# Kernel optimization log

Measured on AMD Instinct MI355X. Metric: run time of the kernel, lower is better.

## Reference

```python
import jax, jax.numpy as jnp
import numpy as np

N_EMBD = 1024
N_HEAD = 16
HEAD = N_EMBD // N_HEAD
D_FF = 4 * N_EMBD
B, T = 2, 2048


def setup_inputs() -> dict:
    key = jax.random.key(0)
    ks = jax.random.split(key, 12)
    s = 0.02
    return {
        "x": jax.random.normal(ks[0], (B, T, N_EMBD), jnp.float32),
        "Wq": jax.random.normal(ks[1], (N_EMBD, N_EMBD), jnp.float32) * s,
        "bq": jnp.zeros((N_EMBD,), jnp.float32),
        "Wk": jax.random.normal(ks[2], (N_EMBD, N_EMBD), jnp.float32) * s,
        "bk": jnp.zeros((N_EMBD,), jnp.float32),
        "Wv": jax.random.normal(ks[3], (N_EMBD, N_EMBD), jnp.float32) * s,
        "bv": jnp.zeros((N_EMBD,), jnp.float32),
        "Wo": jax.random.normal(ks[4], (N_EMBD, N_EMBD), jnp.float32) * s,
        "bo": jnp.zeros((N_EMBD,), jnp.float32),
        "W1": jax.random.normal(ks[5], (N_EMBD, D_FF), jnp.float32) * s,
        "b1": jnp.zeros((D_FF,), jnp.float32),
        "W2": jax.random.normal(ks[6], (D_FF, N_EMBD), jnp.float32) * s,
        "b2": jnp.zeros((N_EMBD,), jnp.float32),
        "g1": jnp.ones((N_EMBD,), jnp.float32),
        "be1": jnp.zeros((N_EMBD,), jnp.float32),
        "g2": jnp.ones((N_EMBD,), jnp.float32),
        "be2": jnp.zeros((N_EMBD,), jnp.float32),
    }


def _layernorm(x, g, b, eps=1e-3):
    # keras LayerNormalization default epsilon=1e-3
    mu = jnp.mean(x, axis=-1, keepdims=True)
    var = jnp.mean(jnp.square(x - mu), axis=-1, keepdims=True)
    return (x - mu) * jax.lax.rsqrt(var + eps) * g + b


def _attention(h, Wq, bq, Wk, bk, Wv, bv, Wo, bo):
    b, t, _ = h.shape
    q = (h @ Wq + bq).reshape(b, t, N_HEAD, HEAD)
    k = (h @ Wk + bk).reshape(b, t, N_HEAD, HEAD)
    v = (h @ Wv + bv).reshape(b, t, N_HEAD, HEAD)
    scores = jnp.einsum("bthd,bshd->bhts", q, k) / jnp.sqrt(jnp.float32(HEAD))
    causal = jnp.tril(jnp.ones((t, t), bool))
    scores = jnp.where(causal, scores, -jnp.inf)
    w = jax.nn.softmax(scores, axis=-1)  # dropout is identity in eval
    ctx = jnp.einsum("bhts,bshd->bthd", w, v).reshape(b, t, N_EMBD)
    return ctx @ Wo + bo


def reference(x, Wq, bq, Wk, bk, Wv, bv, Wo, bo, W1, b1, W2, b2, g1, be1, g2, be2):
    x = x + _attention(_layernorm(x, g1, be1), Wq, bq, Wk, bk, Wv, bv, Wo, bo)
    h = _layernorm(x, g2, be2)
    ff = jax.nn.relu(h @ W1 + b1) @ W2 + b2
    return x + ff
```

## Files before the change

### kernel.cpp

```cpp
#include <hip/hip_runtime.h>

typedef __bf16 bf16;
typedef __attribute__((ext_vector_type(8))) __bf16 bf16x8;
typedef __attribute__((ext_vector_type(4))) __bf16 bf16x4;
typedef __attribute__((ext_vector_type(4))) float f32x4;

#define MFMA16(A, B, C) __builtin_amdgcn_mfma_f32_16x16x32_bf16(A, B, C, 0, 0, 0)

#define GLOAD16(gp, lp)                                          \
  __builtin_amdgcn_global_load_lds(                              \
      (const __attribute__((address_space(1))) void*)(gp),       \
      (__attribute__((address_space(3))) void*)(lp), 16, 0, 0)

__device__ __forceinline__ float fexp2(float x) {
#if __has_builtin(__builtin_amdgcn_exp2f)
  return __builtin_amdgcn_exp2f(x);
#else
  float r;
  asm("v_exp_f32 %0, %1" : "=v"(r) : "v"(x));
  return r;
#endif
}

#define QSCL 0.18033688011112042f

__global__ __launch_bounds__(256) void transpose_cvt_kernel(
    const float* __restrict__ in, bf16* __restrict__ out, int K, int N)
{
  __shared__ float tile[32][33];
  const int kt = blockIdx.y * 32;
  const int nt = blockIdx.x * 32;
  const int tx = threadIdx.x, ty = threadIdx.y;
#pragma unroll
  for (int j = 0; j < 4; ++j)
    tile[ty + j * 8][tx] = in[(size_t)(kt + ty + j * 8) * N + nt + tx];
  __syncthreads();
#pragma unroll
  for (int j = 0; j < 4; ++j)
    out[(size_t)(nt + ty + j * 8) * K + kt + tx] = (bf16)tile[tx][ty + j * 8];
}

__global__ __launch_bounds__(256) void ln_kernel(
    const float* __restrict__ in, const float* __restrict__ gamma,
    const float* __restrict__ beta, bf16* __restrict__ out)
{
  const int row = blockIdx.x;
  const int t = threadIdx.x;
  const float4 v = ((const float4*)(in + (size_t)row * 1024))[t];
  float s = v.x + v.y + v.z + v.w;
  float sq = v.x * v.x + v.y * v.y + v.z * v.z + v.w * v.w;
#pragma unroll
  for (int m = 1; m < 64; m <<= 1) {
    s += __shfl_xor(s, m);
    sq += __shfl_xor(sq, m);
  }
  __shared__ float ssum[4], ssq[4];
  const int w = t >> 6;
  if ((t & 63) == 0) { ssum[w] = s; ssq[w] = sq; }
  __syncthreads();
  s = ssum[0] + ssum[1] + ssum[2] + ssum[3];
  sq = ssq[0] + ssq[1] + ssq[2] + ssq[3];
  const float mu = s * (1.0f / 1024.0f);
  const float var = sq * (1.0f / 1024.0f) - mu * mu;
  const float rs = rsqrtf(var + 1e-3f);
  const float4 g = ((const float4*)gamma)[t];
  const float4 b = ((const float4*)beta)[t];
  bf16x4 o;
  o[0] = (bf16)((v.x - mu) * rs * g.x + b.x);
  o[1] = (bf16)((v.y - mu) * rs * g.y + b.y);
  o[2] = (bf16)((v.z - mu) * rs * g.z + b.z);
  o[3] = (bf16)((v.w - mu) * rs * g.w + b.w);
  *(bf16x4*)(out + (size_t)row * 1024 + t * 4) = o;
}

template <int BN, int BK, int EPI>
__global__ __launch_bounds__(256) void gemm_bt(
    const bf16* __restrict__ A, const bf16* __restrict__ Bt,
    const float* __restrict__ bias0, const float* __restrict__ bias1,
    const float* __restrict__ bias2, const float* __restrict__ resid,
    bf16* __restrict__ out0, bf16* __restrict__ out1, bf16* __restrict__ out2,
    float* __restrict__ outf, int M, int N, int K)
{
  constexpr int WN = BN / 2;
  constexpr int NJ = WN / 16;
  constexpr int KK = BK / 32;
  constexpr int NSLOT = BK / 8;
  constexpr int SMASK = NSLOT - 1;
  constexpr int RPL = 512 / BK;
  constexpr int ALOADS = 128 / (4 * RPL);
  constexpr int BLOADS = BN / (4 * RPL);
  constexpr int S = ALOADS + BLOADS;

  __shared__ bf16 As[3][128 * BK];
  __shared__ bf16 Bs[3][BN * BK];
  const int tid = threadIdx.x;
  const int lane = tid & 63, w = tid >> 6;
  const int wr = w >> 1, wc = w & 1;
  const int g = lane >> 4, lr = lane & 15;
  const int brow = blockIdx.y * 128, bcol = blockIdx.x * BN;

  f32x4 acc[4][NJ] = {};

  const int lrow = lane / NSLOT;
  const int slot = lane & SMASK;
  const int lcol = (slot ^ (lrow & SMASK)) * 8;

  auto stage = [&](int buf, int k0) {
#pragma unroll
    for (int j = 0; j < ALOADS; ++j) {
      const int row0 = w * 32 + j * RPL;
      GLOAD16(A + (size_t)(brow + row0 + lrow) * K + k0 + lcol,
              &As[buf][row0 * BK]);
    }
#pragma unroll
    for (int j = 0; j < BLOADS; ++j) {
      const int row0 = w * (BN / 4) + j * RPL;
      GLOAD16(Bt + (size_t)(bcol + row0 + lrow) * K + k0 + lcol,
              &Bs[buf][row0 * BK]);
    }
  };

  const int nk = K / BK;
  stage(0, 0);
  stage(1, BK);
  int cur = 0;
  for (int t = 0; t < nk; ++t) {
    if (t + 1 < nk) {
      if constexpr (S == 3)
        asm volatile("s_waitcnt vmcnt(3)" ::: "memory");
      else if constexpr (S == 4)
        asm volatile("s_waitcnt vmcnt(4)" ::: "memory");
      else
        asm volatile("s_waitcnt vmcnt(6)" ::: "memory");
    } else {
      asm volatile("s_waitcnt vmcnt(0)" ::: "memory");
    }
    __builtin_amdgcn_s_barrier();
    __builtin_amdgcn_sched_barrier(0);

    bf16x8 afr[4][KK], bfr[NJ][KK];
#pragma unroll
    for (int i = 0; i < 4; ++i)
#pragma unroll
      for (int kk = 0; kk < KK; ++kk)
        afr[i][kk] = *(const bf16x8*)&As[cur][(wr * 64 + i * 16 + lr) * BK +
                                             (((kk * 4 + g) ^ (lr & SMASK)) * 8)];
#pragma unroll
    for (int j = 0; j < NJ; ++j)
#pragma unroll
      for (int kk = 0; kk < KK; ++kk)
        bfr[j][kk] = *(const bf16x8*)&Bs[cur][(wc * WN + j * 16 + lr) * BK +
                                             (((kk * 4 + g) ^ (lr & SMASK)) * 8)];

    if (t + 2 < nk) {
      int nb = cur + 2;
      if (nb >= 3) nb -= 3;
      stage(nb, (t + 2) * BK);
    }

    __builtin_amdgcn_s_setprio(1);
#pragma unroll
    for (int kk = 0; kk < KK; ++kk)
#pragma unroll
      for (int i = 0; i < 4; ++i)
#pragma unroll
        for (int j = 0; j < NJ; ++j)
          acc[i][j] = MFMA16(afr[i][kk], bfr[j][kk], acc[i][j]);
    __builtin_amdgcn_s_setprio(0);

    ++cur;
    if (cur == 3) cur = 0;
  }

#pragma unroll
  for (int i = 0; i < 4; ++i) {
#pragma unroll
    for (int j = 0; j < NJ; ++j) {
      const int r0 = brow + wr * 64 + i * 16 + g * 4;
      const int c = bcol + wc * WN + j * 16 + lr;
      if constexpr (EPI == 1) {
        const float bv = bias0[c];
#pragma unroll
        for (int rr = 0; rr < 4; ++rr)
          out0[(size_t)(r0 + rr) * N + c] = (bf16)fmaxf(acc[i][j][rr] + bv, 0.0f);
      } else if constexpr (EPI == 2) {
        const float bv = bias0[c];
#pragma unroll
        for (int rr = 0; rr < 4; ++rr) {
          const size_t idx = (size_t)(r0 + rr) * N + c;
          outf[idx] = acc[i][j][rr] + bv + resid[idx];
        }
      } else {
        const int sub = c >> 10;
        const int c1 = c & 1023;
        if (sub == 0) {
          const float bv = bias0[c1];
#pragma unroll
          for (int rr = 0; rr < 4; ++rr)
            out0[(size_t)(r0 + rr) * 1024 + c1] =
                (bf16)((acc[i][j][rr] + bv) * QSCL);
        } else if (sub == 1) {
          const float bv = bias1[c1];
#pragma unroll
          for (int rr = 0; rr < 4; ++rr)
            out1[(size_t)(r0 + rr) * 1024 + c1] = (bf16)(acc[i][j][rr] + bv);
        } else {
          const float bv = bias2[c1];
          const int bb = r0 >> 11, t0 = r0 & 2047;
          const int hh = c1 >> 6, dd = c1 & 63;
          bf16x4 pk;
#pragma unroll
          for (int rr = 0; rr < 4; ++rr) pk[rr] = (bf16)(acc[i][j][rr] + bv);
          *(bf16x4*)(out2 + ((size_t)((bb * 16 + hh) * 64 + dd)) * 2048 + t0) = pk;
        }
      }
    }
  }
}

__global__ __launch_bounds__(256) void attn_kernel(
    const bf16* __restrict__ q, const bf16* __restrict__ kmat,
    const bf16* __restrict__ vt, bf16* __restrict__ ctx)
{
  __shared__ bf16 Ks[64 * 64];
  __shared__ bf16 Vs[64 * 64];
  __shared__ bf16 Pq[4][16][88];
  const int bx = blockIdx.x, by = blockIdx.y;
  const int qt = (by & 16) ? (31 - ((bx + by - 16) & 31)) : ((bx + by) & 31);
  const int b_ = by >> 4, h_ = by & 15;
  const int qb = qt * 64;
  const int tid = threadIdx.x;
  const int lane = tid & 63, w = tid >> 6;
  const int g = lane >> 4, lr = lane & 15;
  const int qrow = qb + w * 16 + lr;

  bf16x8 qf[2];
  {
    const bf16* qp = q + (size_t)(b_ * 2048 + qrow) * 1024 + h_ * 64 + g * 8;
    qf[0] = *(const bf16x8*)qp;
    qf[1] = *(const bf16x8*)(qp + 32);
  }

  f32x4 o[4] = {};
  float m = -1e30f, l = 0.f;

  const int srow = tid >> 2;
  const int c16 = (tid & 3) * 16;
  const int rb = srow * 128;
  const int sw = (srow & 7) << 4;
  const bf16* kbase = kmat + (size_t)(b_ * 2048) * 1024 + h_ * 64;
  const bf16* vbase = vt + (size_t)(b_ * 16 + h_) * 64 * 2048;
  const bf16* kp0 = kbase + (size_t)srow * 1024 + c16;
  const bf16* vp0 = vbase + (size_t)srow * 2048 + c16;

  bf16x8 k0 = *(const bf16x8*)kp0;
  bf16x8 k1 = *(const bf16x8*)(kp0 + 8);
  bf16x8 v0 = *(const bf16x8*)vp0;
  bf16x8 v1 = *(const bf16x8*)(vp0 + 8);

  for (int s0 = 0; s0 <= qb; s0 += 64) {
    *(bf16x8*)((char*)Ks + ((rb + c16 * 2) ^ sw)) = k0;
    *(bf16x8*)((char*)Ks + ((rb + c16 * 2 + 16) ^ sw)) = k1;
    *(bf16x8*)((char*)Vs + ((rb + c16 * 2) ^ sw)) = v0;
    *(bf16x8*)((char*)Vs + ((rb + c16 * 2 + 16) ^ sw)) = v1;
    __syncthreads();
    if (s0 < qb) {
      const bf16* kp = kp0 + (size_t)(s0 + 64) * 1024;
      k0 = *(const bf16x8*)kp;
      k1 = *(const bf16x8*)(kp + 8);
      const bf16* vp = vp0 + (s0 + 64);
      v0 = *(const bf16x8*)vp;
      v1 = *(const bf16x8*)(vp + 8);
    }

    f32x4 st[4];
#pragma unroll
    for (int n = 0; n < 4; ++n) {
      f32x4 z = {};
#pragma unroll
      for (int kk = 0; kk < 2; ++kk) {
        const int row = n * 16 + lr;
        bf16x8 ak = *(const bf16x8*)((char*)Ks +
            ((row * 128 + kk * 64 + g * 16) ^ ((lr & 7) << 4)));
        z = MFMA16(ak, qf[kk], z);
      }
      st[n] = z;
    }

    if (s0 == qb) {
#pragma unroll
      for (int n = 0; n < 4; ++n)
#pragma unroll
        for (int r = 0; r < 4; ++r)
          if (s0 + n * 16 + g * 4 + r > qrow) st[n][r] = -1e30f;
    }

    float pm = -1e30f;
#pragma unroll
    for (int n = 0; n < 4; ++n)
#pragma unroll
      for (int r = 0; r < 4; ++r) pm = fmaxf(pm, st[n][r]);
    pm = fmaxf(pm, __shfl_xor(pm, 16));
    pm = fmaxf(pm, __shfl_xor(pm, 32));

    if (__any(pm > m + 8.0f)) {
      const float mn = fmaxf(m, pm);
      const float alpha = fexp2(m - mn);
      m = mn;
      l *= alpha;
      float av[4];
#pragma unroll
      for (int r = 0; r < 4; ++r) av[r] = __shfl(alpha, g * 4 + r);
#pragma unroll
      for (int n = 0; n < 4; ++n)
#pragma unroll
        for (int r = 0; r < 4; ++r) o[n][r] *= av[r];
    }

    float rs = 0.f;
#pragma unroll
    for (int n = 0; n < 4; ++n) {
      bf16x4 pk;
#pragma unroll
      for (int r = 0; r < 4; ++r) {
        const float p = fexp2(st[n][r] - m);
        rs += p;
        pk[r] = (bf16)p;
      }
      *(bf16x4*)&Pq[w][lr][n * 16 + g * 4] = pk;
    }
    rs += __shfl_xor(rs, 16);
    rs += __shfl_xor(rs, 32);
    l += rs;

    bf16x8 pa[2];
#pragma unroll
    for (int kk = 0; kk < 2; ++kk)
      pa[kk] = *(const bf16x8*)&Pq[w][lr][kk * 32 + g * 8];
#pragma unroll
    for (int n = 0; n < 4; ++n) {
      const int row = n * 16 + lr;
#pragma unroll
      for (int kk = 0; kk < 2; ++kk) {
        bf16x8 bv = *(const bf16x8*)((char*)Vs +
            ((row * 128 + kk * 64 + g * 16) ^ ((lr & 7) << 4)));
        o[n] = MFMA16(pa[kk], bv, o[n]);
      }
    }
    __syncthreads();
  }

  float lq[4];
#pragma unroll
  for (int r = 0; r < 4; ++r) lq[r] = __shfl(l, g * 4 + r);
#pragma unroll
  for (int r = 0; r < 4; ++r) {
    const float inv = 1.0f / lq[r];
#pragma unroll
    for (int n = 0; n < 4; ++n)
      ctx[(size_t)(b_ * 2048 + qb + w * 16 + g * 4 + r) * 1024 + h_ * 64 + n * 16 + lr] =
          (bf16)(o[n][r] * inv);
  }
}

extern "C" void kernel_launch(void* const* d_in, const int* in_sizes, int n_in,
                              void* d_out, int out_size, void* d_ws, size_t ws_size,
                              hipStream_t stream)
{
  (void)in_sizes; (void)n_in; (void)out_size; (void)ws_size;
  const float* x   = (const float*)d_in[0];
  const float* Wq  = (const float*)d_in[1];
  const float* bq  = (const float*)d_in[2];
  const float* Wk  = (const float*)d_in[3];
  const float* bk  = (const float*)d_in[4];
  const float* Wv  = (const float*)d_in[5];
  const float* bv  = (const float*)d_in[6];
  const float* Wo  = (const float*)d_in[7];
  const float* bo  = (const float*)d_in[8];
  const float* W1  = (const float*)d_in[9];
  const float* b1  = (const float*)d_in[10];
  const float* W2  = (const float*)d_in[11];
  const float* b2  = (const float*)d_in[12];
  const float* g1  = (const float*)d_in[13];
  const float* be1 = (const float*)d_in[14];
  const float* g2  = (const float*)d_in[15];
  const float* be2 = (const float*)d_in[16];
  float* out = (float*)d_out;

  char* ws = (char*)d_ws;
  const size_t MB = 1024 * 1024;
  bf16* wqkv_t = (bf16*)(ws + 0 * MB);
  bf16* wq_t = (bf16*)(ws + 0 * MB);
  bf16* wk_t = (bf16*)(ws + 2 * MB);
  bf16* wv_t = (bf16*)(ws + 4 * MB);
  bf16* wo_t = (bf16*)(ws + 6 * MB);
  bf16* w1_t = (bf16*)(ws + 8 * MB);
  bf16* w2_t = (bf16*)(ws + 16 * MB);
  bf16* h1   = (bf16*)(ws + 24 * MB);
  bf16* qbuf = (bf16*)(ws + 32 * MB);
  bf16* kbuf = (bf16*)(ws + 40 * MB);
  bf16* vtb  = (bf16*)(ws + 48 * MB);
  bf16* ctx  = (bf16*)(ws + 56 * MB);
  bf16* h2   = (bf16*)(ws + 64 * MB);
  bf16* ff1  = (bf16*)(ws + 24 * MB);

  const dim3 tb(32, 8);
  transpose_cvt_kernel<<<dim3(32, 32), tb, 0, stream>>>(Wq, wq_t, 1024, 1024);
  transpose_cvt_kernel<<<dim3(32, 32), tb, 0, stream>>>(Wk, wk_t, 1024, 1024);
  transpose_cvt_kernel<<<dim3(32, 32), tb, 0, stream>>>(Wv, wv_t, 1024, 1024);
  transpose_cvt_kernel<<<dim3(32, 32), tb, 0, stream>>>(Wo, wo_t, 1024, 1024);
  transpose_cvt_kernel<<<dim3(128, 32), tb, 0, stream>>>(W1, w1_t, 1024, 4096);
  transpose_cvt_kernel<<<dim3(32, 128), tb, 0, stream>>>(W2, w2_t, 4096, 1024);

  ln_kernel<<<4096, 256, 0, stream>>>(x, g1, be1, h1);

  gemm_bt<128, 32, 4><<<dim3(24, 32), 256, 0, stream>>>(
      h1, wqkv_t, bq, bk, bv, nullptr, qbuf, kbuf, vtb, nullptr, 4096, 3072, 1024);

  attn_kernel<<<dim3(32, 32), 256, 0, stream>>>(qbuf, kbuf, vtb, ctx);

  gemm_bt<64, 64, 2><<<dim3(16, 32), 256, 0, stream>>>(
      ctx, wo_t, bo, nullptr, nullptr, x, nullptr, nullptr, nullptr, out, 4096, 1024, 1024);

  ln_kernel<<<4096, 256, 0, stream>>>(out, g2, be2, h2);

  gemm_bt<128, 32, 1><<<dim3(32, 32), 256, 0, stream>>>(
      h2, w1_t, b1, nullptr, nullptr, nullptr, ff1, nullptr, nullptr, nullptr, 4096, 4096, 1024);

  gemm_bt<64, 64, 2><<<dim3(16, 32), 256, 0, stream>>>(
      ff1, w2_t, b2, nullptr, nullptr, out, nullptr, nullptr, nullptr, out, 4096, 1024, 4096);
}
```

Baseline: 225.5 us.

## Add 256x256-tile 512-thread GEMM for QKV and FFN1 projections

Adds a new GEMM kernel with 256x256 output tiles, 8 waves, BK=64, double-buffered LDS staging with an XOR swizzle, and an MFMA schedule split into four phases. It replaces the 128-wide gemm_bt for the QKV projection and the first FFN matmul, and the old gemm_bt is trimmed to only the residual epilogue. Larger tiles raise arithmetic intensity and cut global/LDS traffic per flop. The cost is high register use (128 accumulator floats per thread), fewer blocks (192 and 256 on a 256-CU part), and possible wave-quantization or occupancy losses.

```diff
diff --git a/kernel.cpp b/kernel.cpp
--- a/kernel.cpp
+++ b/kernel.cpp
@@ -73,12 +73,165 @@
   *(bf16x4*)(out + (size_t)row * 1024 + t * 4) = o;
 }
 
+template <int EPI>
+__global__ __launch_bounds__(512, 2) void gemm256(
+    const bf16* __restrict__ A, const bf16* __restrict__ Bt,
+    const float* __restrict__ bias0, const float* __restrict__ bias1,
+    const float* __restrict__ bias2,
+    bf16* __restrict__ out0, bf16* __restrict__ out1, bf16* __restrict__ out2,
+    int M, int N, int K)
+{
+  __shared__ bf16 As[2][256 * 64];
+  __shared__ bf16 Bs[2][256 * 64];
+  const int tid = threadIdx.x;
+  const int lane = tid & 63, w = tid >> 6;
+  const int wr = w >> 2, wc = w & 3;
+  const int g = lane >> 4, lr = lane & 15;
+  const int brow = blockIdx.y * 256, bcol = blockIdx.x * 256;
+
+  f32x4 acc[8][4] = {};
+
+  const int srow = lane >> 3;
+  const int scol = ((lane & 7) ^ srow) * 8;
+
+  auto stage_all = [&](int buf, int k0) {
+#pragma unroll
+    for (int c = 0; c < 4; ++c) {
+      const int r0 = c * 64 + w * 8;
+      GLOAD16(A + (size_t)(brow + r0 + srow) * K + k0 + scol,
+              &As[buf][r0 * 64]);
+    }
+#pragma unroll
+    for (int c = 0; c < 4; ++c) {
+      const int r0 = c * 64 + w * 8;
+      GLOAD16(Bt + (size_t)(bcol + r0 + srow) * K + k0 + scol,
+              &Bs[buf][r0 * 64]);
+    }
+  };
+
+  const int arow = (wr * 128 + lr) * 128;
+  const int brow_ = (wc * 64 + lr) * 128;
+  const int x0 = (g ^ (lr & 7)) * 16;
+  const int x1 = ((4 + g) ^ (lr & 7)) * 16;
+
+  const int nk = K >> 6;
+  stage_all(0, 0);
+  asm volatile("s_waitcnt vmcnt(0)" ::: "memory");
+  __builtin_amdgcn_s_barrier();
+
+  int cur = 0;
+  for (int t = 0; t < nk; ++t) {
+    if (t + 1 < nk) stage_all(cur ^ 1, (t + 1) << 6);
+    __builtin_amdgcn_sched_barrier(0);
+    const char* pA = (const char*)&As[cur][0];
+    const char* pB = (const char*)&Bs[cur][0];
+    bf16x8 a[4], b0[4], b1[4];
+
+#pragma unroll
+    for (int i = 0; i < 4; ++i) a[i] = *(const bf16x8*)(pA + arow + i * 2048 + x0);
+#pragma unroll
+    for (int j = 0; j < 4; ++j) b0[j] = *(const bf16x8*)(pB + brow_ + j * 2048 + x0);
+    __builtin_amdgcn_s_barrier();
+    asm volatile("s_waitcnt lgkmcnt(0)" ::: "memory");
+    __builtin_amdgcn_sched_barrier(0);
+    __builtin_amdgcn_s_setprio(1);
+#pragma unroll
+    for (int i = 0; i < 4; ++i)
+#pragma unroll
+      for (int j = 0; j < 4; ++j) acc[i][j] = MFMA16(a[i], b0[j], acc[i][j]);
+    __builtin_amdgcn_s_setprio(0);
+    __builtin_amdgcn_s_barrier();
+
+#pragma unroll
+    for (int i = 0; i < 4; ++i) a[i] = *(const bf16x8*)(pA + arow + i * 2048 + x1);
+#pragma unroll
+    for (int j = 0; j < 4; ++j) b1[j] = *(const bf16x8*)(pB + brow_ + j * 2048 + x1);
+    __builtin_amdgcn_s_barrier();
+    asm volatile("s_waitcnt lgkmcnt(0)" ::: "memory");
+    __builtin_amdgcn_sched_barrier(0);
+    __builtin_amdgcn_s_setprio(1);
+#pragma unroll
+    for (int i = 0; i < 4; ++i)
+#pragma unroll
+      for (int j = 0; j < 4; ++j) acc[i][j] = MFMA16(a[i], b1[j], acc[i][j]);
+    __builtin_amdgcn_s_setprio(0);
+    __builtin_amdgcn_s_barrier();
+
+#pragma unroll
+    for (int i = 0; i < 4; ++i)
+      a[i] = *(const bf16x8*)(pA + arow + (4 + i) * 2048 + x0);
+    __builtin_amdgcn_s_barrier();
+    asm volatile("s_waitcnt lgkmcnt(0)" ::: "memory");
+    __builtin_amdgcn_sched_barrier(0);
+    __builtin_amdgcn_s_setprio(1);
+#pragma unroll
+    for (int i = 0; i < 4; ++i)
+#pragma unroll
+      for (int j = 0; j < 4; ++j) acc[4 + i][j] = MFMA16(a[i], b0[j], acc[4 + i][j]);
+    __builtin_amdgcn_s_setprio(0);
+    __builtin_amdgcn_s_barrier();
+
+#pragma unroll
+    for (int i = 0; i < 4; ++i)
+      a[i] = *(const bf16x8*)(pA + arow + (4 + i) * 2048 + x1);
+    __builtin_amdgcn_s_barrier();
+    asm volatile("s_waitcnt lgkmcnt(0)" ::: "memory");
+    __builtin_amdgcn_sched_barrier(0);
+    __builtin_amdgcn_s_setprio(1);
+#pragma unroll
+    for (int i = 0; i < 4; ++i)
+#pragma unroll
+      for (int j = 0; j < 4; ++j) acc[4 + i][j] = MFMA16(a[i], b1[j], acc[4 + i][j]);
+    __builtin_amdgcn_s_setprio(0);
+    asm volatile("s_waitcnt vmcnt(0)" ::: "memory");
+    __builtin_amdgcn_s_barrier();
+    cur ^= 1;
+  }
+
+#pragma unroll
+  for (int nj = 0; nj < 4; ++nj) {
+    const int c = bcol + wc * 64 + nj * 16 + lr;
+#pragma unroll
+    for (int mi = 0; mi < 8; ++mi) {
+      const int r0 = brow + wr * 128 + mi * 16 + g * 4;
+      if constexpr (EPI == 1) {
+        const float bv = bias0[c];
+#pragma unroll
+        for (int rr = 0; rr < 4; ++rr)
+          out0[(size_t)(r0 + rr) * N + c] =
+              (bf16)fmaxf(acc[mi][nj][rr] + bv, 0.0f);
+      } else {
+        const int sub = c >> 10;
+        const int c1 = c & 1023;
+        if (sub == 0) {
+          const float bv = bias0[c1];
+#pragma unroll
+          for (int rr = 0; rr < 4; ++rr)
+            out0[(size_t)(r0 + rr) * 1024 + c1] =
+                (bf16)((acc[mi][nj][rr] + bv) * QSCL);
+        } else if (sub == 1) {
+          const float bv = bias1[c1];
+#pragma unroll
+          for (int rr = 0; rr < 4; ++rr)
+            out1[(size_t)(r0 + rr) * 1024 + c1] = (bf16)(acc[mi][nj][rr] + bv);
+        } else {
+          const float bv = bias2[c1];
+          const int bb = r0 >> 11, t0 = r0 & 2047;
+          const int hh = c1 >> 6, dd = c1 & 63;
+          bf16x4 pk;
+#pragma unroll
+          for (int rr = 0; rr < 4; ++rr) pk[rr] = (bf16)(acc[mi][nj][rr] + bv);
+          *(bf16x4*)(out2 + ((size_t)((bb * 16 + hh) * 64 + dd)) * 2048 + t0) = pk;
+        }
+      }
+    }
+  }
+}
+
 template <int BN, int BK, int EPI>
 __global__ __launch_bounds__(256) void gemm_bt(
     const bf16* __restrict__ A, const bf16* __restrict__ Bt,
-    const float* __restrict__ bias0, const float* __restrict__ bias1,
-    const float* __restrict__ bias2, const float* __restrict__ resid,
-    bf16* __restrict__ out0, bf16* __restrict__ out1, bf16* __restrict__ out2,
+    const float* __restrict__ bias0, const float* __restrict__ resid,
     float* __restrict__ outf, int M, int N, int K)
 {
   constexpr int WN = BN / 2;
@@ -178,41 +331,11 @@
     for (int j = 0; j < NJ; ++j) {
       const int r0 = brow + wr * 64 + i * 16 + g * 4;
       const int c = bcol + wc * WN + j * 16 + lr;
-      if constexpr (EPI == 1) {
-        const float bv = bias0[c];
-#pragma unroll
-        for (int rr = 0; rr < 4; ++rr)
-          out0[(size_t)(r0 + rr) * N + c] = (bf16)fmaxf(acc[i][j][rr] + bv, 0.0f);
-      } else if constexpr (EPI == 2) {
-        const float bv = bias0[c];
-#pragma unroll
-        for (int rr = 0; rr < 4; ++rr) {
-          const size_t idx = (size_t)(r0 + rr) * N + c;
-          outf[idx] = acc[i][j][rr] + bv + resid[idx];
-        }
-      } else {
-        const int sub = c >> 10;
-        const int c1 = c & 1023;
-        if (sub == 0) {
-          const float bv = bias0[c1];
-#pragma unroll
-          for (int rr = 0; rr < 4; ++rr)
-            out0[(size_t)(r0 + rr) * 1024 + c1] =
-                (bf16)((acc[i][j][rr] + bv) * QSCL);
-        } else if (sub == 1) {
-          const float bv = bias1[c1];
-#pragma unroll
-          for (int rr = 0; rr < 4; ++rr)
-            out1[(size_t)(r0 + rr) * 1024 + c1] = (bf16)(acc[i][j][rr] + bv);
-        } else {
-          const float bv = bias2[c1];
-          const int bb = r0 >> 11, t0 = r0 & 2047;
-          const int hh = c1 >> 6, dd = c1 & 63;
-          bf16x4 pk;
-#pragma unroll
-          for (int rr = 0; rr < 4; ++rr) pk[rr] = (bf16)(acc[i][j][rr] + bv);
-          *(bf16x4*)(out2 + ((size_t)((bb * 16 + hh) * 64 + dd)) * 2048 + t0) = pk;
-        }
+      const float bv = bias0[c];
+#pragma unroll
+      for (int rr = 0; rr < 4; ++rr) {
+        const size_t idx = (size_t)(r0 + rr) * N + c;
+        outf[idx] = acc[i][j][rr] + bv + resid[idx];
       }
     }
   }
@@ -414,19 +537,19 @@
 
   ln_kernel<<<4096, 256, 0, stream>>>(x, g1, be1, h1);
 
-  gemm_bt<128, 32, 4><<<dim3(24, 32), 256, 0, stream>>>(
-      h1, wqkv_t, bq, bk, bv, nullptr, qbuf, kbuf, vtb, nullptr, 4096, 3072, 1024);
+  gemm256<4><<<dim3(12, 16), 512, 0, stream>>>(
+      h1, wqkv_t, bq, bk, bv, qbuf, kbuf, vtb, 4096, 3072, 1024);
 
   attn_kernel<<<dim3(32, 32), 256, 0, stream>>>(qbuf, kbuf, vtb, ctx);
 
   gemm_bt<64, 64, 2><<<dim3(16, 32), 256, 0, stream>>>(
-      ctx, wo_t, bo, nullptr, nullptr, x, nullptr, nullptr, nullptr, out, 4096, 1024, 1024);
+      ctx, wo_t, bo, x, out, 4096, 1024, 1024);
 
   ln_kernel<<<4096, 256, 0, stream>>>(out, g2, be2, h2);
 
-  gemm_bt<128, 32, 1><<<dim3(32, 32), 256, 0, stream>>>(
-      h2, w1_t, b1, nullptr, nullptr, nullptr, ff1, nullptr, nullptr, nullptr, 4096, 4096, 1024);
+  gemm256<1><<<dim3(16, 16), 512, 0, stream>>>(
+      h2, w1_t, b1, nullptr, nullptr, ff1, nullptr, nullptr, 4096, 4096, 1024);
 
   gemm_bt<64, 64, 2><<<dim3(16, 32), 256, 0, stream>>>(
-      ff1, w2_t, b2, nullptr, nullptr, out, nullptr, nullptr, nullptr, out, 4096, 1024, 4096);
-}
+      ff1, w2_t, b2, out, out, 4096, 1024, 4096);
+}
```

New measurement: 237.8 us. 5.4% more time.
